# Kernel optimization log

Measured on AMD Instinct MI355X. Metric: run time of the kernel, lower is better.

## Reference

```python
import jax, jax.numpy as jnp
import numpy as np

PATCH_SIZE = 14
MERGE_K = 2
HIDDEN = 1024
N_IMAGES = 8
# pixel sizes (H, W) per image; all grid dims (size // patch) are even
PIXEL_SIZES = np.array([
    [1540, 1540], [1120, 1540], [784, 1092], [1540, 868],
    [952, 952], [1260, 1708], [644, 644], [1400, 1400]
], dtype=np.int32)


def setup_inputs() -> dict:
    key = jax.random.key(0)
    k1, k2 = jax.random.split(key)
    grids = PIXEL_SIZES // PATCH_SIZE
    total_tokens = int((grids[:, 0] * grids[:, 1]).sum())  # 59808
    image_features = jax.random.normal(k1, (total_tokens, HIDDEN), dtype=jnp.float32)
    # merging_layer kernel: [in_features, out_features] = [k^2 * d, d], no bias
    W = jax.random.normal(k2, (MERGE_K * MERGE_K * HIDDEN, HIDDEN), dtype=jnp.float32) * 0.02
    image_sizes = jnp.asarray(PIXEL_SIZES)
    return {"image_features": image_features, "image_sizes": image_sizes, "W": W}


def _merge_tokens(image_features, sizes_np, k):
    # sizes_np: static python list of (h, w) patch-grid dims
    d = image_features.shape[-1]
    outs = []
    off = 0
    for h, w in sizes_np:
        n = h * w
        tok = jax.lax.dynamic_slice_in_dim(image_features, off, n, axis=0)  # [h*w, d]
        # [h, w, d] -> [h//k, k, w//k, k, d] -> [h//k, w//k, k, k, d] -> [(h//k)*(w//k), k*k*d]
        g = tok.reshape(h // k, k, w // k, k, d)
        g = g.transpose(0, 2, 1, 3, 4).reshape((h // k) * (w // k), k * k * d)
        outs.append(g)
        off += n
    return jnp.concatenate(outs, axis=0)


def reference(image_features, image_sizes, W):
    sizes = [(int(h) // PATCH_SIZE, int(w) // PATCH_SIZE) for h, w in np.asarray(image_sizes)]
    merged = _merge_tokens(image_features, sizes, MERGE_K)  # [sum(h*w)/k^2, k^2*d]
    return merged @ W  # [n_merged, d]
```

## Files before the change

kernel.cpp:

```cpp
#include <hip/hip_runtime.h>
#include <hip/hip_bf16.h>
#include <stdint.h>

#define M_TOTAL 14952
#define NDIM    1024
#define KDIM    4096
#define BM      128
#define BN      128
#define BK      32
#define KSTEPS  (KDIM / BK)
#define MBLKS   117
#define AS_STRIDE 40

typedef __bf16 bf16x8 __attribute__((ext_vector_type(8)));
typedef float  f32x4  __attribute__((ext_vector_type(4)));

__device__ __forceinline__ unsigned short bf16_rne(float f) {
    unsigned u = __float_as_uint(f);
    u += 0x7FFFu + ((u >> 16) & 1u);
    return (unsigned short)(u >> 16);
}
__device__ __forceinline__ unsigned pack2_rne(float a, float b) {
    return (unsigned)bf16_rne(a) | ((unsigned)bf16_rne(b) << 16);
}
__device__ __forceinline__ unsigned pack_bf16_trunc(float a, float b) {
    return (__float_as_uint(a) >> 16) | (__float_as_uint(b) & 0xFFFF0000u);
}

__global__ void repack_w_kernel(const float* __restrict__ W,
                                unsigned short* __restrict__ Wp) {
    const int nb = blockIdx.x & 7;
    const int ks = blockIdx.x >> 3;
    const int t = threadIdx.x;
    const int n = t & 127;
    const int kqh = t >> 7;
    unsigned short* chunk = Wp + (size_t)(nb * KSTEPS + ks) * (BK * BN);
#pragma unroll
    for (int kq2 = 0; kq2 < 2; ++kq2) {
        const int kq = kqh * 2 + kq2;
        const float* src = W + (size_t)(ks * 32 + kq * 8) * NDIM + nb * 128 + n;
        float f[8];
#pragma unroll
        for (int k7 = 0; k7 < 8; ++k7) f[k7] = src[(size_t)k7 * NDIM];
        uint4 pk;
        pk.x = pack2_rne(f[0], f[1]);
        pk.y = pack2_rne(f[2], f[3]);
        pk.z = pack2_rne(f[4], f[5]);
        pk.w = pack2_rne(f[6], f[7]);
        *(uint4*)(chunk + kq * 1024 + n * 8) = pk;
    }
}

__global__ void gather_a_kernel(const float* __restrict__ feat,
                                unsigned short* __restrict__ Aw) {
    const int p = blockIdx.x;
    const int mb = blockIdx.y;
    const int t = threadIdx.x;
    const int mloc = t >> 1;
    const int half = t & 1;
    int m = mb * 128 + mloc;
    if (m >= M_TOTAL) m = 0;

    const int merged_off[8] = {0, 3025, 5225, 6317, 8022, 9178, 11923, 12452};
    const int tok_off[8]    = {0, 12100, 20900, 25268, 32088, 36712, 47692, 49808};
    const int gw_arr[8]     = {110, 110, 78, 62, 68, 122, 46, 100};
    const int mw_arr[8]     = {55, 55, 39, 31, 34, 61, 23, 50};
    int local = 0, gw = 110, mwv = 55, toff = 0;
#pragma unroll
    for (int i = 0; i < 8; ++i)
        if (m >= merged_off[i]) {
            local = m - merged_off[i];
            gw = gw_arr[i]; mwv = mw_arr[i]; toff = tok_off[i];
        }
    const int ii = local / mwv;
    const int jj = local - ii * mwv;
    const int srcrow = toff + 2 * ii * gw + 2 * jj + (p >> 1) * gw + (p & 1);

    const float* src = feat + (size_t)srcrow * NDIM + half * 512;
    unsigned short* dst = Aw + (((size_t)(mb * 128 + p * 32 + half * 16)) << 12)
                        + mloc * 8;
#pragma unroll 4
    for (int c8 = 0; c8 < 64; ++c8) {
        float4 f0 = *(const float4*)(src + c8 * 8);
        float4 f1 = *(const float4*)(src + c8 * 8 + 4);
        uint4 pk;
        pk.x = pack2_rne(f0.x, f0.y);
        pk.y = pack2_rne(f0.z, f0.w);
        pk.z = pack2_rne(f1.x, f1.y);
        pk.w = pack2_rne(f1.z, f1.w);
        *(uint4*)(dst + (size_t)c8 * 1024) = pk;
    }
}

__global__ __launch_bounds__(256, 2) void gemm2_kernel(
    const unsigned short* __restrict__ Aw,
    const unsigned short* __restrict__ Wp,
    float* __restrict__ out) {

    __shared__ __align__(16) unsigned short As[4096];
    __shared__ __align__(16) unsigned short Bs[4096];

    const int t = threadIdx.x;
    const int lane = t & 63;
    const int wave = t >> 6;
    const int wave_m = (wave >> 1) * 64;
    const int wave_n = (wave & 1) * 64;
    const int nb = blockIdx.x;
    const int mb = blockIdx.y;

    const unsigned short* achunk = Aw + ((size_t)mb * 128) * 4096 + wave * 1024 + lane * 8;
    const unsigned short* wchunk = Wp + ((size_t)nb * 128) * 4096 + wave * 1024 + lane * 8;

    const int ln = lane & 15;
    const int quad = lane >> 4;

    f32x4 acc[4][4];
#pragma unroll
    for (int i = 0; i < 4; ++i)
#pragma unroll
        for (int j = 0; j < 4; ++j) {
            f32x4 z = {0.f, 0.f, 0.f, 0.f};
            acc[i][j] = z;
        }

    for (int ks = 0; ks < KSTEPS; ++ks) {
        const unsigned short* asrc = achunk + (size_t)ks * 4096;
        const unsigned short* bsrc = wchunk + (size_t)ks * 4096;
        __builtin_amdgcn_global_load_lds(
            (const __attribute__((address_space(1))) unsigned int*)asrc,
            (__attribute__((address_space(3))) unsigned int*)&As[wave * 1024], 16, 0, 0);
        __builtin_amdgcn_global_load_lds(
            (const __attribute__((address_space(1))) unsigned int*)(asrc + 512),
            (__attribute__((address_space(3))) unsigned int*)&As[wave * 1024 + 512], 16, 0, 0);
        __builtin_amdgcn_global_load_lds(
            (const __attribute__((address_space(1))) unsigned int*)bsrc,
            (__attribute__((address_space(3))) unsigned int*)&Bs[wave * 1024], 16, 0, 0);
        __builtin_amdgcn_global_load_lds(
            (const __attribute__((address_space(1))) unsigned int*)(bsrc + 512),
            (__attribute__((address_space(3))) unsigned int*)&Bs[wave * 1024 + 512], 16, 0, 0);

        __syncthreads();

        bf16x8 af[4], bf[4];
#pragma unroll
        for (int mi = 0; mi < 4; ++mi)
            af[mi] = *(const bf16x8*)&As[quad * 1024 + (wave_m + mi * 16 + ln) * 8];
#pragma unroll
        for (int ni = 0; ni < 4; ++ni)
            bf[ni] = *(const bf16x8*)&Bs[quad * 1024 + (wave_n + ni * 16 + ln) * 8];
#pragma unroll
        for (int mi = 0; mi < 4; ++mi)
#pragma unroll
            for (int ni = 0; ni < 4; ++ni)
                acc[mi][ni] = __builtin_amdgcn_mfma_f32_16x16x32_bf16(
                    af[mi], bf[ni], acc[mi][ni], 0, 0, 0);

        __syncthreads();
    }

#pragma unroll
    for (int mi = 0; mi < 4; ++mi) {
#pragma unroll
        for (int rr = 0; rr < 4; ++rr) {
            const int row = mb * BM + wave_m + mi * 16 + quad * 4 + rr;
            if (row < M_TOTAL) {
                float* orow = out + (size_t)row * NDIM + nb * BN + wave_n + ln;
#pragma unroll
                for (int ni = 0; ni < 4; ++ni)
                    orow[ni * 16] = acc[mi][ni][rr];
            }
        }
    }
}

__global__ __launch_bounds__(256, 2) void merger_gemm_kernel(
    const float* __restrict__ feat,
    const unsigned short* __restrict__ Wp,
    float* __restrict__ out) {

    __shared__ __align__(16) unsigned short As[BM * AS_STRIDE];
    __shared__ __align__(16) unsigned short Bs[4 * BN * 8];

    const int t = threadIdx.x;
    const int lane = t & 63;
    const int wave = t >> 6;
    const int wave_m = (wave >> 1) * 64;
    const int wave_n = (wave & 1) * 64;
    const int m0 = blockIdx.x * BM;
    const int n0 = blockIdx.y * BN;

    const int r = t >> 1;
    const int half = t & 1;
    int m = m0 + r;
    if (m >= M_TOTAL) m = 0;

    const int merged_off[8] = {0, 3025, 5225, 6317, 8022, 9178, 11923, 12452};
    const int tok_off[8]    = {0, 12100, 20900, 25268, 32088, 36712, 47692, 49808};
    const int gw_arr[8]     = {110, 110, 78, 62, 68, 122, 46, 100};
    const int mw_arr[8]     = {55, 55, 39, 31, 34, 61, 23, 50};

    int local = 0, gw = 110, mwv = 55, toff = 0;
#pragma unroll
    for (int i = 0; i < 8; ++i) {
        if (m >= merged_off[i]) {
            local = m - merged_off[i];
            gw = gw_arr[i]; mwv = mw_arr[i]; toff = tok_off[i];
        }
    }
    const int ii = local / mwv;
    const int jj = local - ii * mwv;
    const int base = toff + 2 * ii * gw + 2 * jj;
    const float* aptr0 = feat + (size_t)base * NDIM + half * 16;
    const float* aptr1 = feat + (size_t)(base + 1) * NDIM + half * 16;
    const float* aptr2 = feat + (size_t)(base + gw) * NDIM + half * 16;
    const float* aptr3 = feat + (size_t)(base + gw + 1) * NDIM + half * 16;

    unsigned short* as_dst = &As[r * AS_STRIDE + half * 16];
    const unsigned short* wchunk = Wp + (size_t)blockIdx.y * KSTEPS * (BK * BN);

    f32x4 acc[4][4];
#pragma unroll
    for (int i = 0; i < 4; ++i)
#pragma unroll
        for (int j = 0; j < 4; ++j) {
            f32x4 z = {0.f, 0.f, 0.f, 0.f};
            acc[i][j] = z;
        }

    const int ln = lane & 15;
    const int quad = lane >> 4;

#pragma unroll
    for (int p = 0; p < 4; ++p) {
        const float* ap = (p == 0) ? aptr0 : (p == 1) ? aptr1 : (p == 2) ? aptr2 : aptr3;
        for (int ki = 0; ki < 32; ++ki) {
            const int ks = p * 32 + ki;
            const float* src = ap + ki * 32;
            float4 f0 = *(const float4*)(src + 0);
            float4 f1 = *(const float4*)(src + 4);
            float4 f2 = *(const float4*)(src + 8);
            float4 f3 = *(const float4*)(src + 12);
            uint4 p0, p1;
            p0.x = pack_bf16_trunc(f0.x, f0.y);
            p0.y = pack_bf16_trunc(f0.z, f0.w);
            p0.z = pack_bf16_trunc(f1.x, f1.y);
            p0.w = pack_bf16_trunc(f1.z, f1.w);
            p1.x = pack_bf16_trunc(f2.x, f2.y);
            p1.y = pack_bf16_trunc(f2.z, f2.w);
            p1.z = pack_bf16_trunc(f3.x, f3.y);
            p1.w = pack_bf16_trunc(f3.z, f3.w);
            *(uint4*)as_dst = p0;
            *((uint4*)as_dst + 1) = p1;

            const unsigned short* wc = wchunk + (size_t)ks * (BK * BN) + wave * 1024 + lane * 8;
            __builtin_amdgcn_global_load_lds(
                (const __attribute__((address_space(1))) unsigned int*)wc,
                (__attribute__((address_space(3))) unsigned int*)&Bs[wave * 1024], 16, 0, 0);
            __builtin_amdgcn_global_load_lds(
                (const __attribute__((address_space(1))) unsigned int*)(wc + 512),
                (__attribute__((address_space(3))) unsigned int*)&Bs[wave * 1024 + 512], 16, 0, 0);

            __syncthreads();

            bf16x8 af[4], bf[4];
#pragma unroll
            for (int mi = 0; mi < 4; ++mi)
                af[mi] = *(const bf16x8*)&As[(wave_m + mi * 16 + ln) * AS_STRIDE + quad * 8];
#pragma unroll
            for (int ni = 0; ni < 4; ++ni)
                bf[ni] = *(const bf16x8*)&Bs[quad * 1024 + (wave_n + ni * 16 + ln) * 8];
#pragma unroll
            for (int mi = 0; mi < 4; ++mi)
#pragma unroll
                for (int ni = 0; ni < 4; ++ni)
                    acc[mi][ni] = __builtin_amdgcn_mfma_f32_16x16x32_bf16(
                        af[mi], bf[ni], acc[mi][ni], 0, 0, 0);

            __syncthreads();
        }
    }

#pragma unroll
    for (int mi = 0; mi < 4; ++mi) {
#pragma unroll
        for (int rr = 0; rr < 4; ++rr) {
            const int row = m0 + wave_m + mi * 16 + quad * 4 + rr;
            if (row < M_TOTAL) {
                float* orow = out + (size_t)row * NDIM + n0 + wave_n + ln;
#pragma unroll
                for (int ni = 0; ni < 4; ++ni)
                    orow[ni * 16] = acc[mi][ni][rr];
            }
        }
    }
}

extern "C" void kernel_launch(void* const* d_in, const int* in_sizes, int n_in,
                              void* d_out, int out_size, void* d_ws, size_t ws_size,
                              hipStream_t stream) {
    const float* feat = (const float*)d_in[0];
    const float* W = (const float*)d_in[2];
    float* out = (float*)d_out;

    const size_t A_BYTES = (size_t)MBLKS * 128 * 8192;
    const size_t W_BYTES = (size_t)8 * KSTEPS * 8192;

    if (ws_size >= A_BYTES + W_BYTES) {
        unsigned short* Aw = (unsigned short*)d_ws;
        unsigned short* Wp = (unsigned short*)((char*)d_ws + A_BYTES);
        repack_w_kernel<<<1024, 256, 0, stream>>>(W, Wp);
        gather_a_kernel<<<dim3(4, MBLKS), 256, 0, stream>>>(feat, Aw);
        gemm2_kernel<<<dim3(8, MBLKS), 256, 0, stream>>>(Aw, Wp, out);
    } else {
        unsigned short* Wp = (unsigned short*)d_ws;
        repack_w_kernel<<<1024, 256, 0, stream>>>(W, Wp);
        merger_gemm_kernel<<<dim3(MBLKS, 8), 256, 0, stream>>>(feat, Wp, out);
    }
}
```

Baseline: 546.1 us.

## Coalesce gather reads and double GEMM K-step per barrier

Rewrites the gather kernel so each group of 16 lanes reads contiguous 512-byte spans of a source row, instead of each thread streaming its own 2KB half-row. The grid doubles to split the columns. The GEMM loop now loads two 32-wide K chunks into LDS that is twice as large per iteration. This halves the number of __syncthreads barriers and gives more MFMA work per sync, at the cost of more LDS use, which may lower occupancy.

```diff
diff --git a/kernel.cpp b/kernel.cpp
--- a/kernel.cpp
+++ b/kernel.cpp
@@ -7,8 +7,7 @@
 #define KDIM    4096
 #define BM      128
 #define BN      128
-#define BK      32
-#define KSTEPS  (KDIM / BK)
+#define KSTEPS  128
 #define MBLKS   117
 #define AS_STRIDE 40
 
@@ -34,7 +33,7 @@
     const int t = threadIdx.x;
     const int n = t & 127;
     const int kqh = t >> 7;
-    unsigned short* chunk = Wp + (size_t)(nb * KSTEPS + ks) * (BK * BN);
+    unsigned short* chunk = Wp + (size_t)(nb * KSTEPS + ks) * 4096;
 #pragma unroll
     for (int kq2 = 0; kq2 < 2; ++kq2) {
         const int kq = kqh * 2 + kq2;
@@ -51,44 +50,54 @@
     }
 }
 
-__global__ void gather_a_kernel(const float* __restrict__ feat,
-                                unsigned short* __restrict__ Aw) {
-    const int p = blockIdx.x;
+__global__ __launch_bounds__(256) void gather_a_kernel(
+    const float* __restrict__ feat, unsigned short* __restrict__ Aw) {
+    const int bx = blockIdx.x;
+    const int p = bx >> 1;
+    const int jh = bx & 1;
     const int mb = blockIdx.y;
     const int t = threadIdx.x;
-    const int mloc = t >> 1;
-    const int half = t & 1;
-    int m = mb * 128 + mloc;
-    if (m >= M_TOTAL) m = 0;
+    const int w = t >> 6;
+    const int l = t & 63;
+    const int rq = l >> 4;
+    const int ln16 = l & 15;
 
     const int merged_off[8] = {0, 3025, 5225, 6317, 8022, 9178, 11923, 12452};
     const int tok_off[8]    = {0, 12100, 20900, 25268, 32088, 36712, 47692, 49808};
     const int gw_arr[8]     = {110, 110, 78, 62, 68, 122, 46, 100};
     const int mw_arr[8]     = {55, 55, 39, 31, 34, 61, 23, 50};
-    int local = 0, gw = 110, mwv = 55, toff = 0;
-#pragma unroll
-    for (int i = 0; i < 8; ++i)
-        if (m >= merged_off[i]) {
-            local = m - merged_off[i];
-            gw = gw_arr[i]; mwv = mw_arr[i]; toff = tok_off[i];
-        }
-    const int ii = local / mwv;
-    const int jj = local - ii * mwv;
-    const int srcrow = toff + 2 * ii * gw + 2 * jj + (p >> 1) * gw + (p & 1);
-
-    const float* src = feat + (size_t)srcrow * NDIM + half * 512;
-    unsigned short* dst = Aw + (((size_t)(mb * 128 + p * 32 + half * 16)) << 12)
-                        + mloc * 8;
-#pragma unroll 4
-    for (int c8 = 0; c8 < 64; ++c8) {
-        float4 f0 = *(const float4*)(src + c8 * 8);
-        float4 f1 = *(const float4*)(src + c8 * 8 + 4);
-        uint4 pk;
-        pk.x = pack2_rne(f0.x, f0.y);
-        pk.y = pack2_rne(f0.z, f0.w);
-        pk.z = pack2_rne(f1.x, f1.y);
-        pk.w = pack2_rne(f1.z, f1.w);
-        *(uint4*)(dst + (size_t)c8 * 1024) = pk;
+
+#pragma unroll
+    for (int it = 0; it < 8; ++it) {
+        const int mloc = w * 4 + rq + it * 16;
+        int m = mb * 128 + mloc;
+        if (m >= M_TOTAL) m = 0;
+
+        int local = 0, gw = 110, mwv = 55, toff = 0;
+#pragma unroll
+        for (int i = 0; i < 8; ++i)
+            if (m >= merged_off[i]) {
+                local = m - merged_off[i];
+                gw = gw_arr[i]; mwv = mw_arr[i]; toff = tok_off[i];
+            }
+        const int ii = local / mwv;
+        const int jj = local - ii * mwv;
+        const int srcrow = toff + 2 * ii * gw + 2 * jj + (p >> 1) * gw + (p & 1);
+        const float* src = feat + (size_t)srcrow * NDIM;
+        unsigned short* dstbase = Aw + ((size_t)(mb * 128 + p * 32)) * 4096
+                                + (ln16 & 3) * 1024 + mloc * 8;
+#pragma unroll
+        for (int j2 = 0; j2 < 4; ++j2) {
+            const int c = ln16 * 8 + (jh * 4 + j2) * 128;
+            float4 f0 = *(const float4*)(src + c);
+            float4 f1 = *(const float4*)(src + c + 4);
+            uint4 pk;
+            pk.x = pack2_rne(f0.x, f0.y);
+            pk.y = pack2_rne(f0.z, f0.w);
+            pk.z = pack2_rne(f1.x, f1.y);
+            pk.w = pack2_rne(f1.z, f1.w);
+            *(uint4*)(dstbase + (size_t)(c >> 5) * 4096) = pk;
+        }
     }
 }
 
@@ -97,8 +106,8 @@
     const unsigned short* __restrict__ Wp,
     float* __restrict__ out) {
 
-    __shared__ __align__(16) unsigned short As[4096];
-    __shared__ __align__(16) unsigned short Bs[4096];
+    __shared__ __align__(16) unsigned short As[8192];
+    __shared__ __align__(16) unsigned short Bs[8192];
 
     const int t = threadIdx.x;
     const int lane = t & 63;
@@ -123,37 +132,43 @@
             acc[i][j] = z;
         }
 
-    for (int ks = 0; ks < KSTEPS; ++ks) {
-        const unsigned short* asrc = achunk + (size_t)ks * 4096;
-        const unsigned short* bsrc = wchunk + (size_t)ks * 4096;
-        __builtin_amdgcn_global_load_lds(
-            (const __attribute__((address_space(1))) unsigned int*)asrc,
-            (__attribute__((address_space(3))) unsigned int*)&As[wave * 1024], 16, 0, 0);
-        __builtin_amdgcn_global_load_lds(
-            (const __attribute__((address_space(1))) unsigned int*)(asrc + 512),
-            (__attribute__((address_space(3))) unsigned int*)&As[wave * 1024 + 512], 16, 0, 0);
-        __builtin_amdgcn_global_load_lds(
-            (const __attribute__((address_space(1))) unsigned int*)bsrc,
-            (__attribute__((address_space(3))) unsigned int*)&Bs[wave * 1024], 16, 0, 0);
-        __builtin_amdgcn_global_load_lds(
-            (const __attribute__((address_space(1))) unsigned int*)(bsrc + 512),
-            (__attribute__((address_space(3))) unsigned int*)&Bs[wave * 1024 + 512], 16, 0, 0);
+    for (int ks2 = 0; ks2 < KSTEPS / 2; ++ks2) {
+        const unsigned short* asrc = achunk + (size_t)ks2 * 8192;
+        const unsigned short* bsrc = wchunk + (size_t)ks2 * 8192;
+#pragma unroll
+        for (int h = 0; h < 2; ++h) {
+            __builtin_amdgcn_global_load_lds(
+                (const __attribute__((address_space(1))) unsigned int*)(asrc + h * 4096),
+                (__attribute__((address_space(3))) unsigned int*)&As[h * 4096 + wave * 1024], 16, 0, 0);
+            __builtin_amdgcn_global_load_lds(
+                (const __attribute__((address_space(1))) unsigned int*)(asrc + h * 4096 + 512),
+                (__attribute__((address_space(3))) unsigned int*)&As[h * 4096 + wave * 1024 + 512], 16, 0, 0);
+            __builtin_amdgcn_global_load_lds(
+                (const __attribute__((address_space(1))) unsigned int*)(bsrc + h * 4096),
+                (__attribute__((address_space(3))) unsigned int*)&Bs[h * 4096 + wave * 1024], 16, 0, 0);
+            __builtin_amdgcn_global_load_lds(
+                (const __attribute__((address_space(1))) unsigned int*)(bsrc + h * 4096 + 512),
+                (__attribute__((address_space(3))) unsigned int*)&Bs[h * 4096 + wave * 1024 + 512], 16, 0, 0);
+        }
 
         __syncthreads();
 
-        bf16x8 af[4], bf[4];
-#pragma unroll
-        for (int mi = 0; mi < 4; ++mi)
-            af[mi] = *(const bf16x8*)&As[quad * 1024 + (wave_m + mi * 16 + ln) * 8];
-#pragma unroll
-        for (int ni = 0; ni < 4; ++ni)
-            bf[ni] = *(const bf16x8*)&Bs[quad * 1024 + (wave_n + ni * 16 + ln) * 8];
-#pragma unroll
-        for (int mi = 0; mi < 4; ++mi)
+#pragma unroll
+        for (int h = 0; h < 2; ++h) {
+            bf16x8 af[4], bf[4];
+#pragma unroll
+            for (int mi = 0; mi < 4; ++mi)
+                af[mi] = *(const bf16x8*)&As[h * 4096 + quad * 1024 + (wave_m + mi * 16 + ln) * 8];
 #pragma unroll
             for (int ni = 0; ni < 4; ++ni)
-                acc[mi][ni] = __builtin_amdgcn_mfma_f32_16x16x32_bf16(
-                    af[mi], bf[ni], acc[mi][ni], 0, 0, 0);
+                bf[ni] = *(const bf16x8*)&Bs[h * 4096 + quad * 1024 + (wave_n + ni * 16 + ln) * 8];
+#pragma unroll
+            for (int mi = 0; mi < 4; ++mi)
+#pragma unroll
+                for (int ni = 0; ni < 4; ++ni)
+                    acc[mi][ni] = __builtin_amdgcn_mfma_f32_16x16x32_bf16(
+                        af[mi], bf[ni], acc[mi][ni], 0, 0, 0);
+        }
 
         __syncthreads();
     }
@@ -216,7 +231,7 @@
     const float* aptr3 = feat + (size_t)(base + gw + 1) * NDIM + half * 16;
 
     unsigned short* as_dst = &As[r * AS_STRIDE + half * 16];
-    const unsigned short* wchunk = Wp + (size_t)blockIdx.y * KSTEPS * (BK * BN);
+    const unsigned short* wchunk = Wp + (size_t)blockIdx.y * KSTEPS * 4096;
 
     f32x4 acc[4][4];
 #pragma unroll
@@ -252,7 +267,7 @@
             *(uint4*)as_dst = p0;
             *((uint4*)as_dst + 1) = p1;
 
-            const unsigned short* wc = wchunk + (size_t)ks * (BK * BN) + wave * 1024 + lane * 8;
+            const unsigned short* wc = wchunk + (size_t)ks * 4096 + wave * 1024 + lane * 8;
             __builtin_amdgcn_global_load_lds(
                 (const __attribute__((address_space(1))) unsigned int*)wc,
                 (__attribute__((address_space(3))) unsigned int*)&Bs[wave * 1024], 16, 0, 0);
@@ -309,7 +324,7 @@
         unsigned short* Aw = (unsigned short*)d_ws;
         unsigned short* Wp = (unsigned short*)((char*)d_ws + A_BYTES);
         repack_w_kernel<<<1024, 256, 0, stream>>>(W, Wp);
-        gather_a_kernel<<<dim3(4, MBLKS), 256, 0, stream>>>(feat, Aw);
+        gather_a_kernel<<<dim3(8, MBLKS), 256, 0, stream>>>(feat, Aw);
         gemm2_kernel<<<dim3(8, MBLKS), 256, 0, stream>>>(Aw, Wp, out);
     } else {
         unsigned short* Wp = (unsigned short*)d_ws;
```

New measurement: 530.6 us. 2.8% less time.
